# Kernel tuning notes

Measured on AMD Instinct MI355X. Metric: run time of the kernel, lower is better.

Reference implementation:

```python
import jax, jax.numpy as jnp
import numpy as np

H, B, F_IN, H1, H21, H22, C = 10, 32768, 4, 1024, 1024, 1024, 2
OBS_X, OBS_Y, RAD = 40.0, 15.0, 6.0


def setup_inputs() -> dict:
    key = jax.random.key(0)
    ks = jax.random.split(key, 12)
    def lin(k, fan_in, shape):
        return jax.random.normal(k, shape, dtype=jnp.float32) / np.sqrt(fan_in)
    inp = {
        "x": jax.random.normal(ks[0], (B, F_IN), dtype=jnp.float32),
        "W1": lin(ks[1], F_IN, (H, F_IN, H1)),
        "b1": jnp.zeros((H, H1), jnp.float32),
        "W21": lin(ks[2], H1, (H, H1, H21)),
        "b21": jnp.zeros((H, H21), jnp.float32),
        "W22": lin(ks[3], H1, (H, H1, H22)),
        "b22": jnp.zeros((H, H22), jnp.float32),
        "W31": lin(ks[4], H21, (H, H21, C)),
        "b31": jnp.zeros((H, C), jnp.float32),
        "W32": lin(ks[5], H22, (H, H22, C)),
        "b32": jnp.zeros((H, C), jnp.float32),
        "wt": jnp.ones((H,), jnp.float32),
        "mean": jnp.zeros((F_IN,), jnp.float32),
        "std": jnp.array([20.0, 10.0, 1.0, 5.0], jnp.float32),
        "sgn": 1,
        "itr": 1,
    }
    return inp


def reference(x, W1, b1, W21, b21, W22, b22, W31, b31, W32, b32, wt, mean, std, sgn, itr):
    # denormalize state: [B, 4] -> px, py, theta, v
    x0 = x * std + mean
    px, py, theta, v = x0[:, 0], x0[:, 1], x0[:, 2], x0[:, 3]
    st, ct = jnp.sin(theta), jnp.cos(theta)
    dx, dy = px - OBS_X, py - OBS_Y

    # barrier function terms (per sample)
    barrier = dx ** 2 + dy ** 2 - RAD ** 2                      # [B]
    barrier_dot = 2.0 * dx * v * ct + 2.0 * dy * v * st         # [B]
    Lf2b = 2.0 * v ** 2                                         # [B]
    LgLfbu1 = -2.0 * dx * v * st + 2.0 * dy * v * ct            # [B]
    LgLfbu2 = 2.0 * dx * ct + 2.0 * dy * st                     # [B]
    G = jnp.stack([-LgLfbu1, -LgLfbu2], axis=1)                 # [B, 2]
    GG = jnp.sum(G * G, axis=1)                                 # [B]

    # all heads at once: [H, B, *]
    h1 = jax.nn.relu(jnp.einsum('bf,hfo->hbo', x, W1) + b1[:, None, :])
    x21 = jax.nn.relu(jnp.einsum('hbo,hop->hbp', h1, W21) + b21[:, None, :])
    x22 = jax.nn.relu(jnp.einsum('hbo,hop->hbp', h1, W22) + b22[:, None, :])
    x31 = jnp.einsum('hbp,hpc->hbc', x21, W31) + b31[:, None, :]          # [H, B, 2]
    x32 = 4.0 * jax.nn.sigmoid(jnp.einsum('hbp,hpc->hbc', x22, W32) + b32[:, None, :])

    # head 0 stores its x32; h-row of QP per head:
    #   i==0: Lf2b + (p1+p2)*bdot + p1*p2*barrier      (p = x32[0])
    #   i>0 : Lf2b + (p1+q1)*bdot + p1*q1*barrier      (q = x32[i])
    p1 = x32[0, :, 0]                                            # [B]
    a = jnp.concatenate([x32[0:1, :, 1], x32[1:, :, 0]], axis=0)  # [H, B]
    h_qp = Lf2b[None, :] + (p1[None, :] + a) * barrier_dot[None, :] \
           + p1[None, :] * a * barrier[None, :]                   # [H, B]

    # QP: min 1/2 u^T u + x31^T u  s.t.  G u <= h  (single row) -> closed form
    z = -x31                                                     # [H, B, 2]
    gz = jnp.einsum('bc,hbc->hb', G, z)                          # [H, B]
    lam = jax.nn.relu(gz - h_qp) / (GG[None, :] + 1e-12)         # [H, B]
    u = z - lam[..., None] * G[None, :, :]                       # [H, B, 2]

    # ensemble weights exp(wt)/sum(exp(wt))
    w = jax.nn.softmax(wt)
    return jnp.einsum('h,hbc->bc', w, u)                          # [B, 2]
```

## Files before the change

### kernel.cpp

```cpp
#include <hip/hip_runtime.h>
#include <hip/hip_bf16.h>
#include <stdint.h>

#define NH 10
#define NB 32768
#define ND 1024

typedef __bf16 bf16x8 __attribute__((ext_vector_type(8)));
typedef float f32x4 __attribute__((ext_vector_type(4)));

typedef const __attribute__((address_space(1))) unsigned int* gas_ptr;
typedef __attribute__((address_space(3))) unsigned int* las_ptr;

__device__ __forceinline__ void load16_lds(const void* g, void* l) {
    __builtin_amdgcn_global_load_lds((gas_ptr)g, (las_ptr)l, 16, 0, 0);
}

__global__ void wt_kernel(const float* __restrict__ W21, const float* __restrict__ W22,
                          __hip_bfloat16* __restrict__ W21T, __hip_bfloat16* __restrict__ W22T) {
    int z = blockIdx.z;
    const float* src;
    __hip_bfloat16* dst;
    if (z < NH) { src = W21 + (size_t)z * ND * ND; dst = W21T + (size_t)z * ND * ND; }
    else        { src = W22 + (size_t)(z - NH) * ND * ND; dst = W22T + (size_t)(z - NH) * ND * ND; }
    int o0 = blockIdx.x * 32, p0 = blockIdx.y * 32;
    __shared__ float tile[32][33];
    int t = threadIdx.x;
    int r = t >> 3, cg = (t & 7) << 2;
    float4 v = *(const float4*)&src[(size_t)(o0 + r) * ND + p0 + cg];
    tile[r][cg + 0] = v.x; tile[r][cg + 1] = v.y; tile[r][cg + 2] = v.z; tile[r][cg + 3] = v.w;
    __syncthreads();
    union { __hip_bfloat16 h[4]; uint2 u; } pk;
#pragma unroll
    for (int i = 0; i < 4; i++) pk.h[i] = __float2bfloat16(tile[cg + i][r]);
    *(uint2*)&dst[(size_t)(p0 + r) * ND + o0 + cg] = pk.u;
}

__global__ void h1_kernel(const float* __restrict__ x, const float* __restrict__ W1,
                          const float* __restrict__ b1, __hip_bfloat16* __restrict__ h1buf,
                          int headBase, int rowBase, int rowsPerIter) {
    int t = threadIdx.x;
    int hl = blockIdx.y;
    int h = headBase + hl;
    int rl = (blockIdx.x << 1) + (t >> 7);
    int b = rowBase + rl;
    int o0 = (t & 127) << 3;
    float4 xv = *(const float4*)&x[(size_t)b * 4];
    const float* xf = (const float*)&xv;
    const float* Wh = W1 + (size_t)h * 4 * ND;
    float acc[8];
    {
        float4 b0 = *(const float4*)&b1[h * ND + o0];
        float4 b4 = *(const float4*)&b1[h * ND + o0 + 4];
        acc[0] = b0.x; acc[1] = b0.y; acc[2] = b0.z; acc[3] = b0.w;
        acc[4] = b4.x; acc[5] = b4.y; acc[6] = b4.z; acc[7] = b4.w;
    }
#pragma unroll
    for (int f = 0; f < 4; f++) {
        float4 w0 = *(const float4*)&Wh[f * ND + o0];
        float4 w4 = *(const float4*)&Wh[f * ND + o0 + 4];
        float s = xf[f];
        acc[0] += s * w0.x; acc[1] += s * w0.y; acc[2] += s * w0.z; acc[3] += s * w0.w;
        acc[4] += s * w4.x; acc[5] += s * w4.y; acc[6] += s * w4.z; acc[7] += s * w4.w;
    }
    union { __hip_bfloat16 hh[8]; uint4 u; } pk;
#pragma unroll
    for (int i = 0; i < 8; i++) {
        float v = acc[i] > 0.f ? acc[i] : 0.f;
        pk.hh[i] = __float2bfloat16(v);
    }
    *(uint4*)&h1buf[((size_t)hl * rowsPerIter + rl) * ND + o0] = pk.u;
}

__global__ __launch_bounds__(256) void gemm_kernel(
    const __hip_bfloat16* __restrict__ h1buf,
    const __hip_bfloat16* __restrict__ W21T, const __hip_bfloat16* __restrict__ W22T,
    const float* __restrict__ b21, const float* __restrict__ b22,
    const float* __restrict__ W31, const float* __restrict__ W32,
    float* __restrict__ Acc31, float* __restrict__ Acc32,
    int headBase, int rowBase, int rowsPerIter) {
    __shared__ __hip_bfloat16 Als[128 * 32];
    __shared__ __hip_bfloat16 Bls[128 * 32];
    __shared__ float red[256];

    const int nt = blockIdx.x;
    const int mt = blockIdx.y;
    const int hl = blockIdx.z;
    const int h = headBase + hl;
    const bool is21 = nt < 8;
    const int ncol0 = (nt & 7) << 7;
    const int tid = threadIdx.x;
    const int lane = tid & 63;
    const int wid = tid >> 6;
    const int wr = wid >> 1, wc = wid & 1;

    const char* Abase = (const char*)(h1buf + ((size_t)hl * rowsPerIter + (size_t)mt * 128) * ND);
    const __hip_bfloat16* WTsel = (is21 ? W21T : W22T) + (size_t)h * ND * ND + (size_t)ncol0 * ND;
    const char* Bbase = (const char*)WTsel;

    f32x4 acc[4][4];
#pragma unroll
    for (int m = 0; m < 4; m++)
#pragma unroll
        for (int n = 0; n < 4; n++) acc[m][n] = (f32x4){0.f, 0.f, 0.f, 0.f};

    const int sg_row = (wid * 32) + (lane >> 2);
    const int sg_off = (lane & 3) * 16;
    char* AlsW = (char*)Als + wid * 2048;
    char* BlsW = (char*)Bls + wid * 2048;

    for (int k = 0; k < ND; k += 32) {
        const char* as = Abase + (size_t)sg_row * 2048 + k * 2 + sg_off;
        const char* bs = Bbase + (size_t)sg_row * 2048 + k * 2 + sg_off;
        load16_lds(as, AlsW);
        load16_lds(as + 16 * 2048, AlsW + 1024);
        load16_lds(bs, BlsW);
        load16_lds(bs + 16 * 2048, BlsW + 1024);
        __syncthreads();
        bf16x8 af[4], bfr[4];
        const char* Ar = (const char*)Als + ((wr * 64 + (lane & 15)) * 64) + ((lane >> 4) * 16);
        const char* Br = (const char*)Bls + ((wc * 64 + (lane & 15)) * 64) + ((lane >> 4) * 16);
#pragma unroll
        for (int m = 0; m < 4; m++) af[m] = *(const bf16x8*)(Ar + m * 16 * 64);
#pragma unroll
        for (int n = 0; n < 4; n++) bfr[n] = *(const bf16x8*)(Br + n * 16 * 64);
#pragma unroll
        for (int m = 0; m < 4; m++)
#pragma unroll
            for (int n = 0; n < 4; n++)
                acc[m][n] = __builtin_amdgcn_mfma_f32_16x16x32_bf16(af[m], bfr[n], acc[m][n], 0, 0, 0);
        __syncthreads();
    }

    red[tid] = 0.f;
    __syncthreads();
    const float* b2 = (is21 ? b21 : b22) + h * ND + ncol0;
    const float* W3 = (is21 ? W31 : W32) + h * ND * 2 + ncol0 * 2;
    float bias[4], w3a[4], w3b[4];
#pragma unroll
    for (int n = 0; n < 4; n++) {
        int cl = wc * 64 + n * 16 + (lane & 15);
        bias[n] = b2[cl];
        w3a[n] = W3[cl * 2 + 0];
        w3b[n] = W3[cl * 2 + 1];
    }
#pragma unroll
    for (int m = 0; m < 4; m++) {
#pragma unroll
        for (int j = 0; j < 4; j++) {
            float s0 = 0.f, s1 = 0.f;
#pragma unroll
            for (int n = 0; n < 4; n++) {
                float v = acc[m][n][j] + bias[n];
                v = v > 0.f ? v : 0.f;
                s0 += v * w3a[n];
                s1 += v * w3b[n];
            }
            s0 += __shfl_xor(s0, 1); s0 += __shfl_xor(s0, 2);
            s0 += __shfl_xor(s0, 4); s0 += __shfl_xor(s0, 8);
            s1 += __shfl_xor(s1, 1); s1 += __shfl_xor(s1, 2);
            s1 += __shfl_xor(s1, 4); s1 += __shfl_xor(s1, 8);
            if ((lane & 15) == 0) {
                int rl = wr * 64 + m * 16 + ((lane >> 4) << 2) + j;
                atomicAdd(&red[rl * 2 + 0], s0);
                atomicAdd(&red[rl * 2 + 1], s1);
            }
        }
    }
    __syncthreads();
    float* Acc = (is21 ? Acc31 : Acc32) + ((size_t)h * NB + rowBase + (size_t)mt * 128) * 2;
    atomicAdd(&Acc[tid], red[tid]);
}

__global__ void final_kernel(const float* __restrict__ x,
                             const float* __restrict__ Acc31, const float* __restrict__ Acc32,
                             const float* __restrict__ b31, const float* __restrict__ b32,
                             const float* __restrict__ wt, const float* __restrict__ mean,
                             const float* __restrict__ stdv, float* __restrict__ out) {
    int b = blockIdx.x * 256 + threadIdx.x;
    float4 xv = *(const float4*)&x[(size_t)b * 4];
    float px = xv.x * stdv[0] + mean[0];
    float py = xv.y * stdv[1] + mean[1];
    float th = xv.z * stdv[2] + mean[2];
    float v  = xv.w * stdv[3] + mean[3];
    float st = sinf(th), ct = cosf(th);
    float dx = px - 40.f, dy = py - 15.f;
    float barrier = dx * dx + dy * dy - 36.f;
    float bdot = 2.f * dx * v * ct + 2.f * dy * v * st;
    float Lf2b = 2.f * v * v;
    float L1 = -2.f * dx * v * st + 2.f * dy * v * ct;
    float L2 = 2.f * dx * ct + 2.f * dy * st;
    float G0 = -L1, G1 = -L2;
    float GG = G0 * G0 + G1 * G1;

    float wv[NH];
    float mx = -1e30f;
#pragma unroll
    for (int h = 0; h < NH; h++) { wv[h] = wt[h]; mx = wv[h] > mx ? wv[h] : mx; }
    float ssum = 0.f;
#pragma unroll
    for (int h = 0; h < NH; h++) { wv[h] = expf(wv[h] - mx); ssum += wv[h]; }
    float winv = 1.f / ssum;

    float out0 = 0.f, out1 = 0.f, p1 = 0.f;
#pragma unroll
    for (int h = 0; h < NH; h++) {
        float2 a31 = *(const float2*)&Acc31[((size_t)h * NB + b) * 2];
        float2 a32 = *(const float2*)&Acc32[((size_t)h * NB + b) * 2];
        float x31_0 = a31.x + b31[h * 2 + 0];
        float x31_1 = a31.y + b31[h * 2 + 1];
        float s0 = 4.f / (1.f + expf(-(a32.x + b32[h * 2 + 0])));
        float a;
        if (h == 0) {
            p1 = s0;
            a = 4.f / (1.f + expf(-(a32.y + b32[1])));
        } else {
            a = s0;
        }
        float hqp = Lf2b + (p1 + a) * bdot + p1 * a * barrier;
        float z0 = -x31_0, z1 = -x31_1;
        float gz = G0 * z0 + G1 * z1;
        float lam = gz - hqp;
        lam = lam > 0.f ? lam : 0.f;
        lam = lam / (GG + 1e-12f);
        float u0 = z0 - lam * G0, u1 = z1 - lam * G1;
        float w = wv[h] * winv;
        out0 += w * u0;
        out1 += w * u1;
    }
    *(float2*)&out[(size_t)b * 2] = (float2){out0, out1};
}

static inline int imin(int a, int b) { return a < b ? a : b; }

extern "C" void kernel_launch(void* const* d_in, const int* in_sizes, int n_in,
                              void* d_out, int out_size, void* d_ws, size_t ws_size,
                              hipStream_t stream) {
    const float* x    = (const float*)d_in[0];
    const float* W1   = (const float*)d_in[1];
    const float* b1   = (const float*)d_in[2];
    const float* W21  = (const float*)d_in[3];
    const float* b21  = (const float*)d_in[4];
    const float* W22  = (const float*)d_in[5];
    const float* b22  = (const float*)d_in[6];
    const float* W31  = (const float*)d_in[7];
    const float* b31  = (const float*)d_in[8];
    const float* W32  = (const float*)d_in[9];
    const float* b32  = (const float*)d_in[10];
    const float* wt   = (const float*)d_in[11];
    const float* mean = (const float*)d_in[12];
    const float* stdv = (const float*)d_in[13];
    float* out = (float*)d_out;

    char* ws = (char*)d_ws;
    size_t off = 0;
    const size_t WT_bytes = (size_t)NH * ND * ND * 2;
    __hip_bfloat16* W21T = (__hip_bfloat16*)(ws + off); off += WT_bytes;
    __hip_bfloat16* W22T = (__hip_bfloat16*)(ws + off); off += WT_bytes;
    const size_t Acc_bytes = (size_t)NH * NB * 2 * 4;
    float* Acc31 = (float*)(ws + off); off += Acc_bytes;
    float* Acc32 = (float*)(ws + off); off += Acc_bytes;
    __hip_bfloat16* h1buf = (__hip_bfloat16*)(ws + off);
    size_t avail = (ws_size > off) ? (ws_size - off) : 0;

    const size_t perHead = (size_t)NB * ND * 2;
    int headsPerIter, rowsPerIter;
    if (avail >= (size_t)NH * perHead) {
        headsPerIter = NH; rowsPerIter = NB;
    } else if (avail >= perHead) {
        headsPerIter = (int)(avail / perHead); rowsPerIter = NB;
    } else {
        headsPerIter = 1;
        size_t rows = (avail / (ND * 2)) & ~(size_t)127;
        rowsPerIter = (int)rows;
        if (rowsPerIter < 128) rowsPerIter = 128;
    }

    hipMemsetAsync(Acc31, 0, Acc_bytes * 2, stream);
    wt_kernel<<<dim3(32, 32, 2 * NH), 256, 0, stream>>>(W21, W22, W21T, W22T);

    for (int h0 = 0; h0 < NH; h0 += headsPerIter) {
        int hs = imin(headsPerIter, NH - h0);
        for (int r0 = 0; r0 < NB; r0 += rowsPerIter) {
            int rows = imin(rowsPerIter, NB - r0);
            h1_kernel<<<dim3(rows / 2, hs), 256, 0, stream>>>(x, W1, b1, h1buf, h0, r0, rowsPerIter);
            gemm_kernel<<<dim3(16, rows / 128, hs), 256, 0, stream>>>(
                h1buf, W21T, W22T, b21, b22, W31, W32, Acc31, Acc32, h0, r0, rowsPerIter);
        }
    }
    final_kernel<<<dim3(NB / 256), 256, 0, stream>>>(x, Acc31, Acc32, b31, b32, wt, mean, stdv, out);
}
```

Measured before the change: 2.072 ms.

## Rewrite second-layer GEMM with 256x256 tiles, double-buffered LDS, swizzle, and XCD remap

The bf16 MFMA GEMM moves from 128x128 tiles with 4 waves and a single LDS buffer to 256x256 tiles with 8 waves. It uses a 128KB double-buffered LDS region loaded with global_load_lds, explicit vmcnt waits and raw s_barriers, so the next K-slice loads while the current one computes. LDS rows are XOR-swizzled to avoid bank conflicts, and a 1D grid is remapped so consecutive tiles spread across XCDs. The aim is more data reuse per tile and hidden memory latency, at the cost of heavy LDS use (one block per CU) and a larger row granularity that rowsPerIter must respect.

```diff
diff --git a/kernel.cpp b/kernel.cpp
--- a/kernel.cpp
+++ b/kernel.cpp
@@ -15,6 +15,10 @@
 __device__ __forceinline__ void load16_lds(const void* g, void* l) {
     __builtin_amdgcn_global_load_lds((gas_ptr)g, (las_ptr)l, 16, 0, 0);
 }
+
+#define BAR() asm volatile("s_barrier" ::: "memory")
+#define WAITV4() asm volatile("s_waitcnt vmcnt(4)" ::: "memory")
+#define WAITV0() asm volatile("s_waitcnt vmcnt(0)" ::: "memory")
 
 __global__ void wt_kernel(const float* __restrict__ W21, const float* __restrict__ W22,
                           __hip_bfloat16* __restrict__ W21T, __hip_bfloat16* __restrict__ W22T) {
@@ -72,80 +76,113 @@
     *(uint4*)&h1buf[((size_t)hl * rowsPerIter + rl) * ND + o0] = pk.u;
 }
 
-__global__ __launch_bounds__(256) void gemm_kernel(
+__global__ __launch_bounds__(512, 2) void gemm_kernel(
     const __hip_bfloat16* __restrict__ h1buf,
     const __hip_bfloat16* __restrict__ W21T, const __hip_bfloat16* __restrict__ W22T,
     const float* __restrict__ b21, const float* __restrict__ b22,
     const float* __restrict__ W31, const float* __restrict__ W32,
     float* __restrict__ Acc31, float* __restrict__ Acc32,
-    int headBase, int rowBase, int rowsPerIter) {
-    __shared__ __hip_bfloat16 Als[128 * 32];
-    __shared__ __hip_bfloat16 Bls[128 * 32];
-    __shared__ float red[256];
-
-    const int nt = blockIdx.x;
-    const int mt = blockIdx.y;
-    const int hl = blockIdx.z;
+    int headBase, int rowBase, int rowsPerIter, int Mtiles) {
+    __shared__ char lds[131072];
+    char* ldsA = lds;
+    char* ldsB = lds + 65536;
+
+    const int t = threadIdx.x;
+    const int lane = t & 63, wid = t >> 6;
+    const int wr = wid >> 2, wc = wid & 3;
+    const int rb = lane & 15;
+
+    const int nblk = gridDim.x;
+    const int orig = blockIdx.x;
+    const int wg = (orig & 7) * (nblk >> 3) + (orig >> 3);
+    const int perHead = Mtiles << 3;
+    const int hl = wg / perHead;
+    const int rem = wg - hl * perHead;
+    const int mt = rem >> 3;
+    const int nt = rem & 7;
     const int h = headBase + hl;
-    const bool is21 = nt < 8;
-    const int ncol0 = (nt & 7) << 7;
-    const int tid = threadIdx.x;
-    const int lane = tid & 63;
-    const int wid = tid >> 6;
-    const int wr = wid >> 1, wc = wid & 1;
-
-    const char* Abase = (const char*)(h1buf + ((size_t)hl * rowsPerIter + (size_t)mt * 128) * ND);
-    const __hip_bfloat16* WTsel = (is21 ? W21T : W22T) + (size_t)h * ND * ND + (size_t)ncol0 * ND;
-    const char* Bbase = (const char*)WTsel;
-
-    f32x4 acc[4][4];
-#pragma unroll
-    for (int m = 0; m < 4; m++)
+    const bool is21 = nt < 4;
+    const int ncol = (nt & 3) << 8;
+
+    const int cswz = ((t & 3) ^ ((t >> 3) & 3)) << 4;
+    const char* Asrc = (const char*)h1buf +
+        (((size_t)hl * rowsPerIter + (size_t)mt * 256 + (t >> 2)) * 2048) + cswz;
+    const __hip_bfloat16* Wsel = is21 ? W21T : W22T;
+    const char* Bsrc = (const char*)Wsel +
+        (((size_t)h * 1024 + ncol + (t >> 2)) * 2048) + cswz;
+
+    const int swz16 = ((lane >> 4) ^ ((rb >> 1) & 3)) << 4;
+    const int aRow = (wr * 128 + rb) * 64 + swz16;
+    const int bRow = (wc * 64 + rb) * 64 + swz16;
+
+    f32x4 acc[8][4];
+#pragma unroll
+    for (int m = 0; m < 8; m++)
 #pragma unroll
         for (int n = 0; n < 4; n++) acc[m][n] = (f32x4){0.f, 0.f, 0.f, 0.f};
-
-    const int sg_row = (wid * 32) + (lane >> 2);
-    const int sg_off = (lane & 3) * 16;
-    char* AlsW = (char*)Als + wid * 2048;
-    char* BlsW = (char*)Bls + wid * 2048;
-
-    for (int k = 0; k < ND; k += 32) {
-        const char* as = Abase + (size_t)sg_row * 2048 + k * 2 + sg_off;
-        const char* bs = Bbase + (size_t)sg_row * 2048 + k * 2 + sg_off;
-        load16_lds(as, AlsW);
-        load16_lds(as + 16 * 2048, AlsW + 1024);
-        load16_lds(bs, BlsW);
-        load16_lds(bs + 16 * 2048, BlsW + 1024);
-        __syncthreads();
-        bf16x8 af[4], bfr[4];
-        const char* Ar = (const char*)Als + ((wr * 64 + (lane & 15)) * 64) + ((lane >> 4) * 16);
-        const char* Br = (const char*)Bls + ((wc * 64 + (lane & 15)) * 64) + ((lane >> 4) * 16);
-#pragma unroll
-        for (int m = 0; m < 4; m++) af[m] = *(const bf16x8*)(Ar + m * 16 * 64);
-#pragma unroll
-        for (int n = 0; n < 4; n++) bfr[n] = *(const bf16x8*)(Br + n * 16 * 64);
-#pragma unroll
-        for (int m = 0; m < 4; m++)
-#pragma unroll
-            for (int n = 0; n < 4; n++)
-                acc[m][n] = __builtin_amdgcn_mfma_f32_16x16x32_bf16(af[m], bfr[n], acc[m][n], 0, 0, 0);
-        __syncthreads();
-    }
-
-    red[tid] = 0.f;
+    bf16x8 af[4], bq[4];
+
+#define GLA(bufb, kh, kt) do { \
+    load16_lds(Asrc + (size_t)(kt) * 128 + (kh) * 64, ldsA + (bufb) * 32768 + (kh) * 16384 + wid * 1024); \
+    load16_lds(Asrc + 262144 + (size_t)(kt) * 128 + (kh) * 64, ldsA + (bufb) * 32768 + (kh) * 16384 + 8192 + wid * 1024); } while (0)
+#define GLB(bufb, kh, kt) do { \
+    load16_lds(Bsrc + (size_t)(kt) * 128 + (kh) * 64, ldsB + (bufb) * 32768 + (kh) * 16384 + wid * 1024); \
+    load16_lds(Bsrc + 262144 + (size_t)(kt) * 128 + (kh) * 64, ldsB + (bufb) * 32768 + (kh) * 16384 + 8192 + wid * 1024); } while (0)
+#define LDB(bufb, ks) { const char* p_ = ldsB + (bufb) * 32768 + (ks) * 16384 + bRow; \
+    bq[0] = *(const bf16x8*)(p_); bq[1] = *(const bf16x8*)(p_ + 1024); \
+    bq[2] = *(const bf16x8*)(p_ + 2048); bq[3] = *(const bf16x8*)(p_ + 3072); }
+#define LDA(bufb, ks, mg) { const char* p_ = ldsA + (bufb) * 32768 + (ks) * 16384 + (mg) * 4096 + aRow; \
+    af[0] = *(const bf16x8*)(p_); af[1] = *(const bf16x8*)(p_ + 1024); \
+    af[2] = *(const bf16x8*)(p_ + 2048); af[3] = *(const bf16x8*)(p_ + 3072); }
+#define FMA16(mg) { \
+    __builtin_amdgcn_s_setprio(1); \
+    _Pragma("unroll") for (int i_ = 0; i_ < 4; ++i_) \
+        _Pragma("unroll") for (int n_ = 0; n_ < 4; ++n_) \
+            acc[(mg) * 4 + i_][n_] = __builtin_amdgcn_mfma_f32_16x16x32_bf16(af[i_], bq[n_], acc[(mg) * 4 + i_][n_], 0, 0, 0); \
+    __builtin_amdgcn_s_setprio(0); }
+
+    GLA(0, 0, 0); GLB(0, 0, 0); GLA(0, 1, 0); GLB(0, 1, 0);
+    WAITV4();
+    BAR();
+
+    int buf = 0;
+    for (int T = 0; T < 15; ++T) {
+        GLA(buf ^ 1, 0, T + 1);
+        LDB(buf, 0); LDA(buf, 0, 0);
+        BAR(); FMA16(0); BAR();
+        GLB(buf ^ 1, 0, T + 1);
+        LDA(buf, 0, 1);
+        WAITV4(); BAR(); FMA16(1); BAR();
+        GLA(buf ^ 1, 1, T + 1);
+        LDB(buf, 1); LDA(buf, 1, 0);
+        BAR(); FMA16(0); BAR();
+        GLB(buf ^ 1, 1, T + 1);
+        LDA(buf, 1, 1);
+        WAITV4(); BAR(); FMA16(1); BAR();
+        buf ^= 1;
+    }
+    LDB(buf, 0); LDA(buf, 0, 0); BAR(); FMA16(0); BAR();
+    LDA(buf, 0, 1); WAITV0(); BAR(); FMA16(1); BAR();
+    LDB(buf, 1); LDA(buf, 1, 0); BAR(); FMA16(0); BAR();
+    LDA(buf, 1, 1); BAR(); FMA16(1); BAR();
+
+    float* red = (float*)lds;
     __syncthreads();
-    const float* b2 = (is21 ? b21 : b22) + h * ND + ncol0;
-    const float* W3 = (is21 ? W31 : W32) + h * ND * 2 + ncol0 * 2;
+    red[t] = 0.f;
+    __syncthreads();
+
+    const float* b2 = (is21 ? b21 : b22) + h * ND + ncol;
+    const float* W3 = (is21 ? W31 : W32) + (size_t)h * ND * 2 + ncol * 2;
     float bias[4], w3a[4], w3b[4];
 #pragma unroll
     for (int n = 0; n < 4; n++) {
-        int cl = wc * 64 + n * 16 + (lane & 15);
+        int cl = wc * 64 + n * 16 + rb;
         bias[n] = b2[cl];
         w3a[n] = W3[cl * 2 + 0];
         w3b[n] = W3[cl * 2 + 1];
     }
 #pragma unroll
-    for (int m = 0; m < 4; m++) {
+    for (int m = 0; m < 8; m++) {
 #pragma unroll
         for (int j = 0; j < 4; j++) {
             float s0 = 0.f, s1 = 0.f;
@@ -160,16 +197,21 @@
             s0 += __shfl_xor(s0, 4); s0 += __shfl_xor(s0, 8);
             s1 += __shfl_xor(s1, 1); s1 += __shfl_xor(s1, 2);
             s1 += __shfl_xor(s1, 4); s1 += __shfl_xor(s1, 8);
-            if ((lane & 15) == 0) {
-                int rl = wr * 64 + m * 16 + ((lane >> 4) << 2) + j;
-                atomicAdd(&red[rl * 2 + 0], s0);
-                atomicAdd(&red[rl * 2 + 1], s1);
+            if (rb == 0) {
+                int row = wr * 128 + m * 16 + ((lane >> 4) << 2) + j;
+                atomicAdd(&red[row * 2 + 0], s0);
+                atomicAdd(&red[row * 2 + 1], s1);
             }
         }
     }
     __syncthreads();
-    float* Acc = (is21 ? Acc31 : Acc32) + ((size_t)h * NB + rowBase + (size_t)mt * 128) * 2;
-    atomicAdd(&Acc[tid], red[tid]);
+    float* Acc = (is21 ? Acc31 : Acc32) + ((size_t)h * NB + rowBase + (size_t)mt * 256) * 2;
+    atomicAdd(&Acc[t], red[t]);
+#undef GLA
+#undef GLB
+#undef LDB
+#undef LDA
+#undef FMA16
 }
 
 __global__ void final_kernel(const float* __restrict__ x,
@@ -271,9 +313,9 @@
         headsPerIter = (int)(avail / perHead); rowsPerIter = NB;
     } else {
         headsPerIter = 1;
-        size_t rows = (avail / (ND * 2)) & ~(size_t)127;
+        size_t rows = (avail / (ND * 2)) & ~(size_t)255;
         rowsPerIter = (int)rows;
-        if (rowsPerIter < 128) rowsPerIter = 128;
+        if (rowsPerIter < 256) rowsPerIter = 256;
     }
 
     hipMemsetAsync(Acc31, 0, Acc_bytes * 2, stream);
@@ -283,9 +325,10 @@
         int hs = imin(headsPerIter, NH - h0);
         for (int r0 = 0; r0 < NB; r0 += rowsPerIter) {
             int rows = imin(rowsPerIter, NB - r0);
+            int Mtiles = rows / 256;
             h1_kernel<<<dim3(rows / 2, hs), 256, 0, stream>>>(x, W1, b1, h1buf, h0, r0, rowsPerIter);
-            gemm_kernel<<<dim3(16, rows / 128, hs), 256, 0, stream>>>(
-                h1buf, W21T, W22T, b21, b22, W31, W32, Acc31, Acc32, h0, r0, rowsPerIter);
+            gemm_kernel<<<dim3(8 * Mtiles * hs), 512, 0, stream>>>(
+                h1buf, W21T, W22T, b21, b22, W31, W32, Acc31, Acc32, h0, r0, rowsPerIter, Mtiles);
         }
     }
     final_kernel<<<dim3(NB / 256), 256, 0, stream>>>(x, Acc31, Acc32, b31, b32, wt, mean, stdv, out);
```

After: 1.724 ms. -16.8%, faster.
